# Kernel optimization log

Hardware: AMD Instinct MI355X
Metric: run time of the kernel (lower is better)

## Reference

```python
import jax, jax.numpy as jnp
import numpy as np

EPS = 1e-5

def channel_norm(x):
    # per-(batch,channel) norm over spatial dims; torch.var default is unbiased (ddof=1)
    mn = x.mean(axis=(-1, -2), keepdims=True)
    std = jnp.sqrt(x.var(axis=(-1, -2), keepdims=True, ddof=1) + EPS)
    return (x - mn) / std

def conv1x1(x, W, b):
    # x: [B,C,H,W], W: [O,C], b: [O]
    return jnp.einsum('oc,bchw->bohw', W, x) + b[None, :, None, None]

def setup_inputs() -> dict:
    key = jax.random.key(0)
    ks = jax.random.split(key, 10)
    B, C, H, W = 4, 512, 64, 64
    s = 1.0 / np.sqrt(C)  # kaiming-uniform-ish scale for 1x1 conv
    inp = {
        'f_c': jax.random.normal(ks[0], (B, C, H, W), jnp.float32),
        'f_s': jax.random.normal(ks[1], (B, C, H, W), jnp.float32),
        'W_c1': jax.random.uniform(ks[2], (C, C), jnp.float32, -s, s),
        'b_c1': jax.random.uniform(ks[3], (C,), jnp.float32, -s, s),
        'W_s1': jax.random.uniform(ks[4], (C, C), jnp.float32, -s, s),
        'b_s1': jax.random.uniform(ks[5], (C,), jnp.float32, -s, s),
        'W_s2': jax.random.uniform(ks[6], (C, C), jnp.float32, -s, s),
        'b_s2': jax.random.uniform(ks[7], (C,), jnp.float32, -s, s),
        'W_csc': jax.random.uniform(ks[8], (C, C), jnp.float32, -s, s),
        'b_csc': jax.random.uniform(ks[9], (C,), jnp.float32, -s, s),
    }
    return inp

def reference(f_c, f_s, W_c1, b_c1, W_s1, b_s1, W_s2, b_s2, W_csc, b_csc):
    B, C, H, W = f_c.shape
    f_c_hat = channel_norm(f_c)
    f_s_hat = channel_norm(f_s)
    f = conv1x1(f_c_hat, W_c1, b_c1).reshape(B, C, H * W)  # queries [B,C,N]
    g = conv1x1(f_s_hat, W_s1, b_s1).reshape(B, C, H * W)  # keys    [B,C,N]
    scores = jnp.einsum('bci,bcj->bij', f, g)              # [B,N,N]
    attention = jax.nn.softmax(scores, axis=-1)
    h = conv1x1(f_s_hat, W_s2, b_s2).reshape(B, C, H * W)  # values  [B,C,N]
    out = jnp.einsum('bcj,bij->bci', h, attention).reshape(B, C, H, W)
    return conv1x1(out, W_csc, b_csc) + f_c
```

## Files before the change

kernel.cpp:

```cpp
#include <hip/hip_runtime.h>

typedef unsigned short u16;
typedef __attribute__((ext_vector_type(8))) _Float16 f16x8;
typedef __attribute__((ext_vector_type(4))) float f32x4;
typedef __attribute__((ext_vector_type(16))) float f32x16;

#define N_SP 4096
#define C_CH 512
#define B_SZ 4

struct PtrTab { u16* p[4]; };

__device__ __forceinline__ u16 f2h(float f) {
    union { _Float16 h; u16 u; } x; x.h = (_Float16)f; return x.u;
}
__device__ __forceinline__ float h2f(u16 u) {
    union { u16 u; _Float16 h; } x; x.u = u; return (float)x.h;
}
__device__ __forceinline__ void async_cp16(const void* g, void* l) {
    __builtin_amdgcn_global_load_lds((const __attribute__((address_space(1))) unsigned*)g,
                                     (__attribute__((address_space(3))) unsigned*)l, 16, 0, 0);
}
__device__ __forceinline__ float wave_reduce_sum(float v) {
    #pragma unroll
    for (int off = 32; off; off >>= 1) v += __shfl_xor(v, off, 64);
    return v;
}
__device__ __forceinline__ float wave_reduce_max(float v) {
    #pragma unroll
    for (int off = 32; off; off >>= 1) v = fmaxf(v, __shfl_xor(v, off, 64));
    return v;
}
__device__ __forceinline__ void bar() { asm volatile("s_barrier" ::: "memory"); }
template<int N> __device__ __forceinline__ void vmwait() {
    if constexpr (N == 0)  asm volatile("s_waitcnt vmcnt(0)" ::: "memory");
    else if constexpr (N == 2)  asm volatile("s_waitcnt vmcnt(2)" ::: "memory");
    else if constexpr (N == 4)  asm volatile("s_waitcnt vmcnt(4)" ::: "memory");
    else if constexpr (N == 6)  asm volatile("s_waitcnt vmcnt(6)" ::: "memory");
    else if constexpr (N == 8)  asm volatile("s_waitcnt vmcnt(8)" ::: "memory");
}
__device__ __forceinline__ void lgkm0() {
    asm volatile("s_waitcnt lgkmcnt(0)" ::: "memory");
    __builtin_amdgcn_sched_barrier(0);
}

__global__ __launch_bounds__(256) void transpose_cast_stats(
        const float* __restrict__ fc, const float* __restrict__ fs,
        u16* __restrict__ xc, u16* __restrict__ xs,
        float* __restrict__ part_s, float* __restrict__ part_ss) {
    __shared__ float tile[64][65];
    const int t = threadIdx.x;
    const int n0 = blockIdx.x * 64, c0 = blockIdx.y * 64;
    const int z = blockIdx.z;
    const int b = z & 3, which = z >> 2;
    const float* src = which ? fs : fc;
    u16* dst = which ? xs : xc;
    const int r = t >> 4, q4 = (t & 15) * 4;
    #pragma unroll
    for (int it = 0; it < 4; ++it) {
        const int row = it * 16 + r;
        float4 v = *(const float4*)(src + ((size_t)b * C_CH + c0 + row) * N_SP + n0 + q4);
        tile[row][q4 + 0] = v.x; tile[row][q4 + 1] = v.y;
        tile[row][q4 + 2] = v.z; tile[row][q4 + 3] = v.w;
    }
    __syncthreads();
    {
        const int cr = t >> 2, q = t & 3;
        float s = 0.f, ss = 0.f;
        #pragma unroll
        for (int i = 0; i < 16; ++i) {
            float a = tile[cr][q * 16 + i];
            s += a; ss += a * a;
        }
        s += __shfl_xor(s, 1, 64);  s += __shfl_xor(s, 2, 64);
        ss += __shfl_xor(ss, 1, 64); ss += __shfl_xor(ss, 2, 64);
        if (q == 0) {
            atomicAdd(&part_s[z * 512 + c0 + cr], s);
            atomicAdd(&part_ss[z * 512 + c0 + cr], ss);
        }
    }
    #pragma unroll
    for (int it = 0; it < 4; ++it) {
        const int nrow = it * 16 + r;
        ushort4 h4;
        h4.x = f2h(tile[q4 + 0][nrow]);
        h4.y = f2h(tile[q4 + 1][nrow]);
        h4.z = f2h(tile[q4 + 2][nrow]);
        h4.w = f2h(tile[q4 + 3][nrow]);
        *(ushort4*)(dst + ((size_t)b * N_SP + n0 + nrow) * C_CH + c0 + q4) = h4;
    }
}

__global__ __launch_bounds__(256) void prep1(
        const float* __restrict__ W_c1, const float* __restrict__ W_s1,
        const float* __restrict__ W_s2, const float* __restrict__ W_csc,
        const float* __restrict__ b_c1, const float* __restrict__ b_s2,
        const float* __restrict__ b_csc,
        u16* __restrict__ Wbase,
        const float* __restrict__ part_s, const float* __restrict__ part_ss,
        float* __restrict__ mu_a, float* __restrict__ rs_a,
        float* __restrict__ w_u, float* __restrict__ bfold0) {
    __shared__ float tile[64][65];
    const int t = threadIdx.x, z = blockIdx.z;
    if (z < 4) {
        const int n0 = blockIdx.x * 64, c0 = blockIdx.y * 64;
        const float* W = (z == 0) ? W_c1 : (z == 1) ? W_s1 : (z == 2) ? W_s2 : W_csc;
        u16* D = Wbase + ((z == 0) ? 2 : (z == 1) ? 0 : (z == 2) ? 3 : 1) * 262144;
        const int r = t >> 4, q4 = (t & 15) * 4;
        #pragma unroll
        for (int it = 0; it < 4; ++it) {
            const int row = it * 16 + r;
            float4 v = *(const float4*)(W + (size_t)(c0 + row) * 512 + n0 + q4);
            if (z == 3) {
                ushort4 h4 = { f2h(v.x), f2h(v.y), f2h(v.z), f2h(v.w) };
                *(ushort4*)(D + (size_t)(c0 + row) * 512 + n0 + q4) = h4;
            } else {
                tile[row][q4 + 0] = v.x; tile[row][q4 + 1] = v.y;
                tile[row][q4 + 2] = v.z; tile[row][q4 + 3] = v.w;
            }
        }
        __syncthreads();
        if (z == 3) return;
        #pragma unroll
        for (int it = 0; it < 4; ++it) {
            const int nrow = it * 16 + r;
            ushort4 h4;
            h4.x = f2h(tile[q4 + 0][nrow]);
            h4.y = f2h(tile[q4 + 1][nrow]);
            h4.z = f2h(tile[q4 + 2][nrow]);
            h4.w = f2h(tile[q4 + 3][nrow]);
            *(ushort4*)(D + (size_t)(n0 + nrow) * 512 + c0 + q4) = h4;
        }
        return;
    }
    const int flat = blockIdx.y * 8 + blockIdx.x;
    if (flat < 8) {
        #pragma unroll
        for (int h = 0; h < 2; ++h) {
            const int c = flat * 512 + h * 256 + t;
            const float S = part_s[c], SS = part_ss[c];
            const float mean = S * (1.f / N_SP);
            const float var = (SS - S * mean) * (1.f / (N_SP - 1));
            mu_a[c] = mean;
            rs_a[c] = rsqrtf(var + 1e-5f);
        }
    } else if (flat < 10) {
        const int d = (flat - 8) * 256 + t;
        float acc = 0.f;
        for (int o = 0; o < 512; ++o) acc += b_c1[o] * W_s1[(size_t)o * 512 + d];
        w_u[d] = acc;
    } else if (flat < 42) {
        const int w4 = t >> 6, l = t & 63;
        #pragma unroll
        for (int q = 0; q < 4; ++q) {
            const int o = (flat - 10) * 16 + w4 * 4 + q;
            const float4 w0 = *(const float4*)(W_csc + (size_t)o * 512 + l * 8);
            const float4 w1 = *(const float4*)(W_csc + (size_t)o * 512 + l * 8 + 4);
            const float4 b0 = *(const float4*)(b_s2 + l * 8);
            const float4 b1 = *(const float4*)(b_s2 + l * 8 + 4);
            float acc = w0.x * b0.x + w0.y * b0.y + w0.z * b0.z + w0.w * b0.w
                      + w1.x * b1.x + w1.y * b1.y + w1.z * b1.z + w1.w * b1.w;
            acc = wave_reduce_sum(acc);
            if (l == 0) bfold0[o] = acc + b_csc[o];
        }
    }
}

__global__ __launch_bounds__(256) void prep2(
        const u16* __restrict__ WqT16, const u16* __restrict__ Wf16,
        const u16* __restrict__ xs,
        const float* __restrict__ mu_a, const float* __restrict__ rs_a,
        const float* __restrict__ bfold0, const float* __restrict__ w_u,
        u16* __restrict__ Wq_z, u16* __restrict__ Wf_z,
        float* __restrict__ bq, float* __restrict__ bh, float* __restrict__ u_) {
    const int id = blockIdx.x, t = threadIdx.x;
    if (id < 1024) {
        const int y = id >> 9;
        const size_t e = ((size_t)(id & 511) * 256 + t) * 8;
        const int z = (int)(e >> 18), rem = (int)(e & 262143);
        const int d = rem >> 9, a0 = rem & 511;
        u16 v[8];
        if (y == 0) {
            *(uint4*)v = *(const uint4*)(WqT16 + rem);
            const float rd = rs_a[(4 + z) * 512 + d];
            const float* rc = rs_a + z * 512 + a0;
            #pragma unroll
            for (int i = 0; i < 8; ++i) v[i] = f2h(h2f(v[i]) * rc[i] * rd);
            *(uint4*)(Wq_z + e) = *(const uint4*)v;
        } else {
            *(uint4*)v = *(const uint4*)(Wf16 + rem);
            const float* rk = rs_a + (4 + z) * 512 + a0;
            #pragma unroll
            for (int i = 0; i < 8; ++i) v[i] = f2h(h2f(v[i]) * rk[i]);
            *(uint4*)(Wf_z + e) = *(const uint4*)v;
        }
    } else if (id < 2048) {
        const int w = t >> 6, l = t & 63;
        const int oid = (id - 1024) * 4 + w;
        const int kind = oid >> 11;
        const int z = (oid >> 9) & 3, d = oid & 511;
        const u16* row = (kind == 0 ? WqT16 : Wf16) + (size_t)d * 512;
        const int sb = (kind == 0 ? z : 4 + z) * 512;
        float acc = 0.f;
        #pragma unroll
        for (int i = 0; i < 8; ++i) {
            const int a = l * 8 + i;
            acc += h2f(row[a]) * mu_a[sb + a] * rs_a[sb + a];
        }
        acc = wave_reduce_sum(acc);
        if (l == 0) {
            if (kind == 0) bq[z * 512 + d] = -acc * rs_a[(4 + z) * 512 + d];
            else           bh[z * 512 + d] = bfold0[d] - acc;
        }
    } else {
        const int id2 = id - 2048;
        const int b = id2 >> 6, xblk = id2 & 63;
        const int w = t >> 6, l = t & 63;
        float4 u0 = *(const float4*)(w_u + l * 8);
        float4 u1 = *(const float4*)(w_u + l * 8 + 4);
        const float4 r0 = *(const float4*)(rs_a + (4 + b) * 512 + l * 8);
        const float4 r1 = *(const float4*)(rs_a + (4 + b) * 512 + l * 8 + 4);
        u0.x *= r0.x; u0.y *= r0.y; u0.z *= r0.z; u0.w *= r0.w;
        u1.x *= r1.x; u1.y *= r1.y; u1.z *= r1.z; u1.w *= r1.w;
        #pragma unroll
        for (int jj = 0; jj < 16; ++jj) {
            const int j = xblk * 64 + w * 16 + jj;
            const u16* row = xs + ((size_t)b * N_SP + j) * C_CH + l * 8;
            f16x8 x = *(const f16x8*)row;
            float acc = (float)x[0] * u0.x + (float)x[1] * u0.y + (float)x[2] * u0.z + (float)x[3] * u0.w
                      + (float)x[4] * u1.x + (float)x[5] * u1.y + (float)x[6] * u1.z + (float)x[7] * u1.w;
            acc = wave_reduce_sum(acc);
            if (l == 0) u_[(size_t)b * N_SP + j] = acc;
        }
    }
}

enum { OUT_F32 = 0, OUT_F16 = 1 };

template<int OUTMODE, bool TABB, bool TABD, int MI, int MJ>
__global__ __launch_bounds__(256) void gemm_bt(
    const u16* __restrict__ A, const u16* __restrict__ B, PtrTab tab,
    float* __restrict__ Df, u16* __restrict__ Dh,
    const float* __restrict__ bias_m, const float* __restrict__ bias_n,
    const float* __restrict__ res,
    int M, int N, int K, int lda, int ldb, int ldd,
    size_t sA, size_t sB, size_t sD, size_t sR, int sBm, int sBn)
{
    constexpr int TM = MI * 64, TN = MJ * 64, BK = 64;
    constexpr int AITS = (TM * BK) / (256 * 8);
    constexpr int BITS = (TN * BK) / (256 * 8);
    __shared__ u16 smem[(TM + TN) * BK];
    u16* As = smem;
    u16* Bs = smem + TM * BK;

    const int t = threadIdx.x;
    const int l = t & 63, w = t >> 6;
    const int m0 = blockIdx.y * TM, n0 = blockIdx.x * TN;
    const size_t zb = blockIdx.z;
    const u16* pA = A + zb * sA + (size_t)m0 * lda;
    const u16* pB = (TABB ? tab.p[zb] : B + zb * sB) + (size_t)n0 * ldb;

    const int wr = (w & 1) * (MI * 32), wc = (w >> 1) * (MJ * 32);

    f32x16 acc[MI][MJ] = {};

    for (int k0 = 0; k0 < K; k0 += BK) {
        #pragma unroll
        for (int it = 0; it < AITS; ++it) {
            const int L = it * 256 + t;
            const int row = L >> 3, c = L & 7;
            const int sc = (c ^ (row & 7)) * 8;
            async_cp16(pA + (size_t)row * lda + k0 + sc, As + L * 8);
        }
        #pragma unroll
        for (int it = 0; it < BITS; ++it) {
            const int L = it * 256 + t;
            const int row = L >> 3, c = L & 7;
            const int sc = (c ^ (row & 7)) * 8;
            async_cp16(pB + (size_t)row * ldb + k0 + sc, Bs + L * 8);
        }
        __syncthreads();
        #pragma unroll
        for (int kk = 0; kk < 4; ++kk) {
            f16x8 af[MI], bf[MJ];
            #pragma unroll
            for (int i = 0; i < MI; ++i) {
                const int row = wr + i * 32 + (l & 31);
                const int ch = ((kk * 2 + (l >> 5)) ^ (row & 7)) * 8;
                af[i] = *(const f16x8*)(As + row * BK + ch);
            }
            #pragma unroll
            for (int j = 0; j < MJ; ++j) {
                const int row = wc + j * 32 + (l & 31);
                const int ch = ((kk * 2 + (l >> 5)) ^ (row & 7)) * 8;
                bf[j] = *(const f16x8*)(Bs + row * BK + ch);
            }
            #pragma unroll
            for (int i = 0; i < MI; ++i)
                #pragma unroll
                for (int j = 0; j < MJ; ++j)
                    acc[i][j] = __builtin_amdgcn_mfma_f32_32x32x16_f16(af[i], bf[j], acc[i][j], 0, 0, 0);
        }
        __syncthreads();
    }

    const int cl = l & 31, rh = (l >> 5) * 4;
    u16* pDh = (OUTMODE == OUT_F16) ? (TABD ? tab.p[zb] : Dh + zb * sD) : nullptr;
    float* pDf = (OUTMODE == OUT_F32) ? (Df + zb * sD) : nullptr;
    #pragma unroll
    for (int i = 0; i < MI; ++i) {
        #pragma unroll
        for (int j = 0; j < MJ; ++j) {
            const int nn = n0 + wc + j * 32 + cl;
            const float bn = bias_n ? bias_n[(size_t)sBn * zb + nn] : 0.f;
            #pragma unroll
            for (int reg = 0; reg < 16; ++reg) {
                const int ml = (reg & 3) + 8 * (reg >> 2) + rh;
                const int mm = m0 + wr + i * 32 + ml;
                float v = acc[i][j][reg] + bn;
                if (bias_m) v += bias_m[(size_t)sBm * zb + mm];
                const size_t off = (size_t)mm * ldd + nn;
                if (OUTMODE == OUT_F32) {
                    if (res) v += res[zb * sR + off];
                    pDf[off] = v;
                } else {
                    pDh[off] = f2h(v);
                }
            }
        }
    }
}

template<int OUTMODE, bool TABB, bool TABD, int BM>
__global__ __launch_bounds__(512, 2) void gemm_f(
    const u16* __restrict__ A, const u16* __restrict__ B, PtrTab tab,
    float* __restrict__ Df, u16* __restrict__ Dh,
    const float* __restrict__ bias_m, const float* __restrict__ bias_n,
    const float* __restrict__ res,
    int K, int lda, int ldb, int ldd,
    size_t sA, size_t sB, size_t sD, size_t sR, int sBm, int sBn)
{
    constexpr int BN = 256, BK = 64;
    constexpr int HM = BM / 2;
    constexpr int MF = BM / 64;
    constexpr int LA = BM / 128;
    constexpr int LB = 2;
    constexpr int LDSH = (BM + BN) * BK;
    __shared__ u16 smem[2 * LDSH];

    const int t = threadIdx.x;
    const int l = t & 63, w = t >> 6;
    const int m0 = blockIdx.y * BM, n0 = blockIdx.x * BN;
    const size_t zb = blockIdx.z;
    const u16* pA = A + zb * sA + (size_t)m0 * lda;
    const u16* pB = (TABB ? tab.p[zb] : B + zb * sB) + (size_t)n0 * ldb;

    const int wr = (w & 1) * (HM / 2);
    const int wc = (w >> 1) * 32;

    f32x4 acc[2 * MF][4] = {};

    auto stageA = [&](int buf, int k0, int half) {
        u16* dst = smem + buf * LDSH;
        #pragma unroll
        for (int it = 0; it < LA; ++it) {
            const int L = it * 512 + t;
            const int row = half * HM + (L >> 3), c = L & 7;
            const int sc = (c ^ (row & 7)) * 8;
            async_cp16(pA + (size_t)row * lda + k0 + sc, dst + row * BK + c * 8);
        }
    };
    auto stageB = [&](int buf, int k0, int half) {
        u16* dst = smem + buf * LDSH + BM * BK;
        #pragma unroll
        for (int it = 0; it < LB; ++it) {
            const int L = it * 512 + t;
            const int row = half * 128 + (L >> 3), c = L & 7;
            const int sc = (c ^ (row & 7)) * 8;
            async_cp16(pB + (size_t)row * ldb + k0 + sc, dst + row * BK + c * 8);
        }
    };
    auto rdA = [&](const u16* As, int qi, int mf, int kk) -> f16x8 {
        const int row = qi * HM + wr + mf * 16 + (l & 15);
        const int ch = (kk * 4 + (l >> 4)) ^ (row & 7);
        return *(const f16x8*)(As + row * BK + ch * 8);
    };
    auto rdB = [&](const u16* Bs, int qj, int nf, int kk) -> f16x8 {
        const int row = qj * 128 + wc + nf * 16 + (l & 15);
        const int ch = (kk * 4 + (l >> 4)) ^ (row & 7);
        return *(const f16x8*)(Bs + row * BK + ch * 8);
    };

    f16x8 af[2][MF][2];
    f16x8 bf[2][2];

    const int NT = K / BK;
    stageA(0, 0, 0); stageA(0, 0, 1); stageB(0, 0, 0); stageB(0, 0, 1);
    vmwait<LB>();
    bar();

    for (int tl = 0; tl < NT; ++tl) {
        const int cur = tl & 1, nxt = cur ^ 1;
        const u16* As = smem + cur * LDSH;
        const u16* Bs = As + BM * BK;
        const int k1 = (tl + 1) * BK;
        const bool pf = (tl + 1 < NT);

        #pragma unroll
        for (int mf = 0; mf < MF; ++mf) { af[0][mf][0] = rdA(As, 0, mf, 0); af[0][mf][1] = rdA(As, 0, mf, 1); }
        #pragma unroll
        for (int nf = 0; nf < 2; ++nf) { bf[nf][0] = rdB(Bs, 0, nf, 0); bf[nf][1] = rdB(Bs, 0, nf, 1); }
        if (pf) stageA(nxt, k1, 0);
        lgkm0();
        __builtin_amdgcn_s_setprio(1);
        #pragma unroll
        for (int mf = 0; mf < MF; ++mf)
            #pragma unroll
            for (int nf = 0; nf < 2; ++nf) {
                acc[mf][nf] = __builtin_amdgcn_mfma_f32_16x16x32_f16(af[0][mf][0], bf[nf][0], acc[mf][nf], 0, 0, 0);
                acc[mf][nf] = __builtin_amdgcn_mfma_f32_16x16x32_f16(af[0][mf][1], bf[nf][1], acc[mf][nf], 0, 0, 0);
            }
        __builtin_amdgcn_s_setprio(0);
        bar();

        #pragma unroll
        for (int mf = 0; mf < MF; ++mf) { af[1][mf][0] = rdA(As, 1, mf, 0); af[1][mf][1] = rdA(As, 1, mf, 1); }
        if (pf) stageA(nxt, k1, 1);
        lgkm0();
        __builtin_amdgcn_s_setprio(1);
        #pragma unroll
        for (int mf = 0; mf < MF; ++mf)
            #pragma unroll
            for (int nf = 0; nf < 2; ++nf) {
                acc[MF + mf][nf] = __builtin_amdgcn_mfma_f32_16x16x32_f16(af[1][mf][0], bf[nf][0], acc[MF + mf][nf], 0, 0, 0);
                acc[MF + mf][nf] = __builtin_amdgcn_mfma_f32_16x16x32_f16(af[1][mf][1], bf[nf][1], acc[MF + mf][nf], 0, 0, 0);
            }
        __builtin_amdgcn_s_setprio(0);
        if (pf) vmwait<2 * LA>(); else vmwait<0>();
        bar();

        #pragma unroll
        for (int nf = 0; nf < 2; ++nf) { bf[nf][0] = rdB(Bs, 1, nf, 0); bf[nf][1] = rdB(Bs, 1, nf, 1); }
        if (pf) stageB(nxt, k1, 0);
        lgkm0();
        __builtin_amdgcn_s_setprio(1);
        #pragma unroll
        for (int mf = 0; mf < MF; ++mf)
            #pragma unroll
            for (int nf = 0; nf < 2; ++nf) {
                acc[MF + mf][2 + nf] = __builtin_amdgcn_mfma_f32_16x16x32_f16(af[1][mf][0], bf[nf][0], acc[MF + mf][2 + nf], 0, 0, 0);
                acc[MF + mf][2 + nf] = __builtin_amdgcn_mfma_f32_16x16x32_f16(af[1][mf][1], bf[nf][1], acc[MF + mf][2 + nf], 0, 0, 0);
            }
        __builtin_amdgcn_s_setprio(0);
        bar();

        if (pf) stageB(nxt, k1, 1);
        __builtin_amdgcn_s_setprio(1);
        #pragma unroll
        for (int mf = 0; mf < MF; ++mf)
            #pragma unroll
            for (int nf = 0; nf < 2; ++nf) {
                acc[mf][2 + nf] = __builtin_amdgcn_mfma_f32_16x16x32_f16(af[0][mf][0], bf[nf][0], acc[mf][2 + nf], 0, 0, 0);
                acc[mf][2 + nf] = __builtin_amdgcn_mfma_f32_16x16x32_f16(af[0][mf][1], bf[nf][1], acc[mf][2 + nf], 0, 0, 0);
            }
        __builtin_amdgcn_s_setprio(0);
        if (pf) vmwait<LB>();
        bar();
    }

    const int cl = l & 15, rh = (l >> 4) * 4;
    u16* pDh = (OUTMODE == OUT_F16) ? (TABD ? tab.p[zb] : Dh + zb * sD) : nullptr;
    float* pDf = (OUTMODE == OUT_F32) ? (Df + zb * sD) : nullptr;
    #pragma unroll
    for (int qi = 0; qi < 2; ++qi) {
        #pragma unroll
        for (int qj = 0; qj < 2; ++qj) {
            #pragma unroll
            for (int mf = 0; mf < MF; ++mf) {
                #pragma unroll
                for (int nf = 0; nf < 2; ++nf) {
                    const int nn = n0 + qj * 128 + wc + nf * 16 + cl;
                    const float bn = bias_n ? bias_n[(size_t)sBn * zb + nn] : 0.f;
                    const f32x4 a4 = acc[qi * MF + mf][qj * 2 + nf];
                    #pragma unroll
                    for (int reg = 0; reg < 4; ++reg) {
                        const int mm = m0 + qi * HM + wr + mf * 16 + rh + reg;
                        float v = a4[reg] + bn;
                        if (bias_m) v += bias_m[(size_t)sBm * zb + mm];
                        const size_t off = (size_t)mm * ldd + nn;
                        if (OUTMODE == OUT_F32) {
                            if (res) v += res[zb * sR + off];
                            pDf[off] = v;
                        } else {
                            pDh[off] = f2h(v);
                        }
                    }
                }
            }
        }
    }
}

__global__ __launch_bounds__(256) void softmax_kernel(PtrTab tab) {
    u16* row = tab.p[blockIdx.y] + (size_t)blockIdx.x * N_SP;
    const int t = threadIdx.x;
    u16 raw[16];
    *(uint4*)(raw + 0) = *(const uint4*)(row + t * 16);
    *(uint4*)(raw + 8) = *(const uint4*)(row + t * 16 + 8);
    float v[16];
    float mx = -1e30f;
    #pragma unroll
    for (int i = 0; i < 16; ++i) { v[i] = h2f(raw[i]); mx = fmaxf(mx, v[i]); }
    mx = wave_reduce_max(mx);
    __shared__ float red[4];
    const int wave = t >> 6;
    if ((t & 63) == 0) red[wave] = mx;
    __syncthreads();
    mx = fmaxf(fmaxf(red[0], red[1]), fmaxf(red[2], red[3]));
    float sum = 0.f;
    #pragma unroll
    for (int i = 0; i < 16; ++i) { v[i] = __expf(v[i] - mx); sum += v[i]; }
    sum = wave_reduce_sum(sum);
    __syncthreads();
    if ((t & 63) == 0) red[wave] = sum;
    __syncthreads();
    const float inv = 1.f / (red[0] + red[1] + red[2] + red[3]);
    #pragma unroll
    for (int i = 0; i < 16; ++i) raw[i] = f2h(v[i] * inv);
    *(uint4*)(row + t * 16)     = *(const uint4*)(raw + 0);
    *(uint4*)(row + t * 16 + 8) = *(const uint4*)(raw + 8);
}

extern "C" void kernel_launch(void* const* d_in, const int* in_sizes, int n_in,
                              void* d_out, int out_size, void* d_ws, size_t ws_size,
                              hipStream_t stream) {
    const float* f_c   = (const float*)d_in[0];
    const float* f_s   = (const float*)d_in[1];
    const float* W_c1  = (const float*)d_in[2];
    const float* b_c1  = (const float*)d_in[3];
    const float* W_s1  = (const float*)d_in[4];
    const float* b_s1  = (const float*)d_in[5]; (void)b_s1;
    const float* W_s2  = (const float*)d_in[6];
    const float* b_s2  = (const float*)d_in[7];
    const float* W_csc = (const float*)d_in[8];
    const float* b_csc = (const float*)d_in[9];

    const size_t PB = (size_t)N_SP * C_CH;
    const size_t M1 = 1024 * 1024;

    u16* ws   = (u16*)d_ws;
    u16* Xs   = ws;
    u16* q_   = ws + 8 * M1;
    u16* hc   = ws + 16 * M1;
    u16* Xc   = ws + 24 * M1;
    u16* S3   = ws + 24 * M1;
    u16* S0   = ws + 40 * M1;
    u16* S1   = ws + 56 * M1;
    u16* S2   = ws + 72 * M1;
    u16* Wbase= ws + 88 * M1;
    u16* WqT16= Wbase + 4 * 262144;
    u16* Wf16 = Wbase + 5 * 262144;
    u16* Wq_z = Wbase + 6 * 262144;
    u16* Wf_z = Wq_z + 1048576;
    float* f32b = (float*)(ws + 92 * M1);
    float* part_s  = f32b;
    float* part_ss = f32b + 4096;
    float* mu_a    = f32b + 8192;
    float* rs_a    = f32b + 12288;
    float* w_u     = f32b + 16384;
    float* bfold0  = f32b + 16896;
    float* bq      = f32b + 17408;
    float* bh      = f32b + 19456;
    float* u_      = f32b + 21504;

    PtrTab Stab; Stab.p[0] = S0; Stab.p[1] = S1; Stab.p[2] = S2; Stab.p[3] = S3;
    PtrTab tab0 = Stab;

    hipMemsetAsync(part_s, 0, 2 * 4096 * sizeof(float), stream);

    transpose_cast_stats<<<dim3(64, 8, 8), 256, 0, stream>>>(f_c, f_s, Xc, Xs, part_s, part_ss);

    prep1<<<dim3(8, 8, 5), 256, 0, stream>>>(W_c1, W_s1, W_s2, W_csc, b_c1, b_s2, b_csc,
                                             Wbase, part_s, part_ss, mu_a, rs_a, w_u, bfold0);

    gemm_bt<OUT_F16, false, false, 2, 2><<<dim3(4, 4, 2), 256, 0, stream>>>(
        Wbase, Wbase + 2 * 262144, tab0, nullptr, WqT16, nullptr, nullptr, nullptr,
        512, 512, 512, 512, 512, 512, 262144, 262144, 262144, 0, 0, 0);

    prep2<<<2304, 256, 0, stream>>>(WqT16, Wf16, Xs, mu_a, rs_a, bfold0, w_u,
                                    Wq_z, Wf_z, bq, bh, u_);

    gemm_f<OUT_F16, false, false, 128><<<dim3(2, 32, B_SZ), 512, 0, stream>>>(
        Xc, Wq_z, tab0, nullptr, q_, nullptr, bq, nullptr,
        C_CH, C_CH, C_CH, C_CH, PB, 262144, PB, 0, 0, 512);
    gemm_f<OUT_F16, false, false, 128><<<dim3(16, 4, B_SZ), 512, 0, stream>>>(
        Wf_z, Xs, tab0, nullptr, hc, bh, nullptr, nullptr,
        C_CH, C_CH, C_CH, N_SP, 262144, PB, PB, 0, 512, 0);

    gemm_f<OUT_F16, false, true, 128><<<dim3(16, 32, B_SZ), 512, 0, stream>>>(
        q_, Xs, Stab, nullptr, nullptr, nullptr, u_, nullptr,
        C_CH, C_CH, C_CH, N_SP, PB, PB, 0, 0, 0, N_SP);

    softmax_kernel<<<dim3(N_SP, B_SZ), 256, 0, stream>>>(Stab);

    gemm_f<OUT_F32, true, false, 128><<<dim3(16, 4, B_SZ), 512, 0, stream>>>(
        hc, nullptr, Stab, (float*)d_out, nullptr, nullptr, nullptr, f_c,
        N_SP, N_SP, N_SP, N_SP, PB, 0, PB, PB, 0, 0);
}
```

Baseline: 448.5 us.

## Add 128x256 GEMM variant for small-M GEMMs and enlarge score GEMM tile

Adds a new gemm_f2 kernel with a 128x256 block tile and a two-phase K loop that reuses A fragments across both column halves of the tile. The Q projection, value projection and final P·V GEMMs now use it. The score GEMM switches to a 256-row M tile, which halves its grid in the M dimension. The aim is more data reuse per block and fewer blocks. The cost is higher register pressure and fewer blocks, which can leave CUs underfilled on the smaller grids.

```diff
diff --git a/kernel.cpp b/kernel.cpp
--- a/kernel.cpp
+++ b/kernel.cpp
@@ -465,6 +465,155 @@
             }
         __builtin_amdgcn_s_setprio(0);
         if (pf) vmwait<LB>();
+        bar();
+    }
+
+    const int cl = l & 15, rh = (l >> 4) * 4;
+    u16* pDh = (OUTMODE == OUT_F16) ? (TABD ? tab.p[zb] : Dh + zb * sD) : nullptr;
+    float* pDf = (OUTMODE == OUT_F32) ? (Df + zb * sD) : nullptr;
+    #pragma unroll
+    for (int qi = 0; qi < 2; ++qi) {
+        #pragma unroll
+        for (int qj = 0; qj < 2; ++qj) {
+            #pragma unroll
+            for (int mf = 0; mf < MF; ++mf) {
+                #pragma unroll
+                for (int nf = 0; nf < 2; ++nf) {
+                    const int nn = n0 + qj * 128 + wc + nf * 16 + cl;
+                    const float bn = bias_n ? bias_n[(size_t)sBn * zb + nn] : 0.f;
+                    const f32x4 a4 = acc[qi * MF + mf][qj * 2 + nf];
+                    #pragma unroll
+                    for (int reg = 0; reg < 4; ++reg) {
+                        const int mm = m0 + qi * HM + wr + mf * 16 + rh + reg;
+                        float v = a4[reg] + bn;
+                        if (bias_m) v += bias_m[(size_t)sBm * zb + mm];
+                        const size_t off = (size_t)mm * ldd + nn;
+                        if (OUTMODE == OUT_F32) {
+                            if (res) v += res[zb * sR + off];
+                            pDf[off] = v;
+                        } else {
+                            pDh[off] = f2h(v);
+                        }
+                    }
+                }
+            }
+        }
+    }
+}
+
+template<int OUTMODE, bool TABB, bool TABD>
+__global__ __launch_bounds__(512, 2) void gemm_f2(
+    const u16* __restrict__ A, const u16* __restrict__ B, PtrTab tab,
+    float* __restrict__ Df, u16* __restrict__ Dh,
+    const float* __restrict__ bias_m, const float* __restrict__ bias_n,
+    const float* __restrict__ res,
+    int K, int lda, int ldb, int ldd,
+    size_t sA, size_t sB, size_t sD, size_t sR, int sBm, int sBn)
+{
+    constexpr int BM = 128, BN = 256, BK = 64;
+    constexpr int HM = 64, MF = 2, LA = 1, LB = 2;
+    constexpr int LDSH = (BM + BN) * BK;
+    __shared__ u16 smem[2 * LDSH];
+
+    const int t = threadIdx.x;
+    const int l = t & 63, w = t >> 6;
+    const int m0 = blockIdx.y * BM, n0 = blockIdx.x * BN;
+    const size_t zb = blockIdx.z;
+    const u16* pA = A + zb * sA + (size_t)m0 * lda;
+    const u16* pB = (TABB ? tab.p[zb] : B + zb * sB) + (size_t)n0 * ldb;
+
+    const int wr = (w & 1) * (HM / 2);
+    const int wc = (w >> 1) * 32;
+
+    f32x4 acc[2 * MF][4] = {};
+
+    auto stageA = [&](int buf, int k0, int half) {
+        u16* dst = smem + buf * LDSH;
+        #pragma unroll
+        for (int it = 0; it < LA; ++it) {
+            const int L = it * 512 + t;
+            const int row = half * HM + (L >> 3), c = L & 7;
+            const int sc = (c ^ (row & 7)) * 8;
+            async_cp16(pA + (size_t)row * lda + k0 + sc, dst + row * BK + c * 8);
+        }
+    };
+    auto stageB = [&](int buf, int k0, int half) {
+        u16* dst = smem + buf * LDSH + BM * BK;
+        #pragma unroll
+        for (int it = 0; it < LB; ++it) {
+            const int L = it * 512 + t;
+            const int row = half * 128 + (L >> 3), c = L & 7;
+            const int sc = (c ^ (row & 7)) * 8;
+            async_cp16(pB + (size_t)row * ldb + k0 + sc, dst + row * BK + c * 8);
+        }
+    };
+    auto rdA = [&](const u16* As, int qi, int mf, int kk) -> f16x8 {
+        const int row = qi * HM + wr + mf * 16 + (l & 15);
+        const int ch = (kk * 4 + (l >> 4)) ^ (row & 7);
+        return *(const f16x8*)(As + row * BK + ch * 8);
+    };
+    auto rdB = [&](const u16* Bs, int qj, int nf, int kk) -> f16x8 {
+        const int row = qj * 128 + wc + nf * 16 + (l & 15);
+        const int ch = (kk * 4 + (l >> 4)) ^ (row & 7);
+        return *(const f16x8*)(Bs + row * BK + ch * 8);
+    };
+
+    f16x8 af[2][MF][2];
+    f16x8 bf[2][2];
+
+    const int NT = K / BK;
+    stageA(0, 0, 0); stageA(0, 0, 1); stageB(0, 0, 0); stageB(0, 0, 1);
+    vmwait<2>();
+    bar();
+
+    for (int tl = 0; tl < NT; ++tl) {
+        const int cur = tl & 1, nxt = cur ^ 1;
+        const u16* As = smem + cur * LDSH;
+        const u16* Bs = As + BM * BK;
+        const int k1 = (tl + 1) * BK;
+        const bool pf = (tl + 1 < NT);
+
+        #pragma unroll
+        for (int qi = 0; qi < 2; ++qi)
+            #pragma unroll
+            for (int mf = 0; mf < MF; ++mf) {
+                af[qi][mf][0] = rdA(As, qi, mf, 0);
+                af[qi][mf][1] = rdA(As, qi, mf, 1);
+            }
+        #pragma unroll
+        for (int nf = 0; nf < 2; ++nf) { bf[nf][0] = rdB(Bs, 0, nf, 0); bf[nf][1] = rdB(Bs, 0, nf, 1); }
+        if (pf) { stageA(nxt, k1, 0); stageA(nxt, k1, 1); stageB(nxt, k1, 0); }
+        lgkm0();
+        __builtin_amdgcn_s_setprio(1);
+        #pragma unroll
+        for (int qi = 0; qi < 2; ++qi)
+            #pragma unroll
+            for (int mf = 0; mf < MF; ++mf)
+                #pragma unroll
+                for (int nf = 0; nf < 2; ++nf) {
+                    acc[qi * MF + mf][nf] = __builtin_amdgcn_mfma_f32_16x16x32_f16(af[qi][mf][0], bf[nf][0], acc[qi * MF + mf][nf], 0, 0, 0);
+                    acc[qi * MF + mf][nf] = __builtin_amdgcn_mfma_f32_16x16x32_f16(af[qi][mf][1], bf[nf][1], acc[qi * MF + mf][nf], 0, 0, 0);
+                }
+        __builtin_amdgcn_s_setprio(0);
+        if (pf) vmwait<4>(); else vmwait<0>();
+        bar();
+
+        #pragma unroll
+        for (int nf = 0; nf < 2; ++nf) { bf[nf][0] = rdB(Bs, 1, nf, 0); bf[nf][1] = rdB(Bs, 1, nf, 1); }
+        if (pf) stageB(nxt, k1, 1);
+        lgkm0();
+        __builtin_amdgcn_s_setprio(1);
+        #pragma unroll
+        for (int qi = 0; qi < 2; ++qi)
+            #pragma unroll
+            for (int mf = 0; mf < MF; ++mf)
+                #pragma unroll
+                for (int nf = 0; nf < 2; ++nf) {
+                    acc[qi * MF + mf][2 + nf] = __builtin_amdgcn_mfma_f32_16x16x32_f16(af[qi][mf][0], bf[nf][0], acc[qi * MF + mf][2 + nf], 0, 0, 0);
+                    acc[qi * MF + mf][2 + nf] = __builtin_amdgcn_mfma_f32_16x16x32_f16(af[qi][mf][1], bf[nf][1], acc[qi * MF + mf][2 + nf], 0, 0, 0);
+                }
+        __builtin_amdgcn_s_setprio(0);
+        if (pf) vmwait<2>();
         bar();
     }
 
@@ -590,20 +739,20 @@
     prep2<<<2304, 256, 0, stream>>>(WqT16, Wf16, Xs, mu_a, rs_a, bfold0, w_u,
                                     Wq_z, Wf_z, bq, bh, u_);
 
-    gemm_f<OUT_F16, false, false, 128><<<dim3(2, 32, B_SZ), 512, 0, stream>>>(
+    gemm_f2<OUT_F16, false, false><<<dim3(2, 32, B_SZ), 512, 0, stream>>>(
         Xc, Wq_z, tab0, nullptr, q_, nullptr, bq, nullptr,
         C_CH, C_CH, C_CH, C_CH, PB, 262144, PB, 0, 0, 512);
-    gemm_f<OUT_F16, false, false, 128><<<dim3(16, 4, B_SZ), 512, 0, stream>>>(
+    gemm_f2<OUT_F16, false, false><<<dim3(16, 4, B_SZ), 512, 0, stream>>>(
         Wf_z, Xs, tab0, nullptr, hc, bh, nullptr, nullptr,
         C_CH, C_CH, C_CH, N_SP, 262144, PB, PB, 0, 512, 0);
 
-    gemm_f<OUT_F16, false, true, 128><<<dim3(16, 32, B_SZ), 512, 0, stream>>>(
+    gemm_f<OUT_F16, false, true, 256><<<dim3(16, 16, B_SZ), 512, 0, stream>>>(
         q_, Xs, Stab, nullptr, nullptr, nullptr, u_, nullptr,
         C_CH, C_CH, C_CH, N_SP, PB, PB, 0, 0, 0, N_SP);
 
     softmax_kernel<<<dim3(N_SP, B_SZ), 256, 0, stream>>>(Stab);
 
-    gemm_f<OUT_F32, true, false, 128><<<dim3(16, 4, B_SZ), 512, 0, stream>>>(
+    gemm_f2<OUT_F32, true, false><<<dim3(16, 4, B_SZ), 512, 0, stream>>>(
         hc, nullptr, Stab, (float*)d_out, nullptr, nullptr, nullptr, f_c,
         N_SP, N_SP, N_SP, N_SP, PB, 0, PB, PB, 0, 0);
 }
```

After: 423.5 us. 5.6% less time.

## Reschedule GEMM main loop with double-buffered B fragments and larger score tile

Applied to the files above, without the earlier changes.

Restructures the MFMA main loop so both A quadrants are read up front and B fragments live in two separate register sets. This removes the explicit lgkmcnt(0) waits and sched barriers, so LDS reads can overlap with MFMA issue, and the vmcnt wait moves to an earlier phase. Separately, the score GEMM now uses a 256-row tile with half as many blocks along M. The costs are higher register pressure and possibly lower occupancy. The earlier vmwait and the new barrier placement also risk subtle LDS ordering issues.

```diff
diff --git a/kernel.cpp b/kernel.cpp
--- a/kernel.cpp
+++ b/kernel.cpp
@@ -34,14 +34,11 @@
 __device__ __forceinline__ void bar() { asm volatile("s_barrier" ::: "memory"); }
 template<int N> __device__ __forceinline__ void vmwait() {
     if constexpr (N == 0)  asm volatile("s_waitcnt vmcnt(0)" ::: "memory");
+    else if constexpr (N == 1)  asm volatile("s_waitcnt vmcnt(1)" ::: "memory");
     else if constexpr (N == 2)  asm volatile("s_waitcnt vmcnt(2)" ::: "memory");
     else if constexpr (N == 4)  asm volatile("s_waitcnt vmcnt(4)" ::: "memory");
     else if constexpr (N == 6)  asm volatile("s_waitcnt vmcnt(6)" ::: "memory");
     else if constexpr (N == 8)  asm volatile("s_waitcnt vmcnt(8)" ::: "memory");
-}
-__device__ __forceinline__ void lgkm0() {
-    asm volatile("s_waitcnt lgkmcnt(0)" ::: "memory");
-    __builtin_amdgcn_sched_barrier(0);
 }
 
 __global__ __launch_bounds__(256) void transpose_cast_stats(
@@ -392,7 +389,8 @@
     };
 
     f16x8 af[2][MF][2];
-    f16x8 bf[2][2];
+    f16x8 bf0[2][2];
+    f16x8 bf1[2][2];
 
     const int NT = K / BK;
     stageA(0, 0, 0); stageA(0, 0, 1); stageB(0, 0, 0); stageB(0, 0, 1);
@@ -409,47 +407,44 @@
         #pragma unroll
         for (int mf = 0; mf < MF; ++mf) { af[0][mf][0] = rdA(As, 0, mf, 0); af[0][mf][1] = rdA(As, 0, mf, 1); }
         #pragma unroll
-        for (int nf = 0; nf < 2; ++nf) { bf[nf][0] = rdB(Bs, 0, nf, 0); bf[nf][1] = rdB(Bs, 0, nf, 1); }
+        for (int nf = 0; nf < 2; ++nf) { bf0[nf][0] = rdB(Bs, 0, nf, 0); bf0[nf][1] = rdB(Bs, 0, nf, 1); }
+        #pragma unroll
+        for (int mf = 0; mf < MF; ++mf) { af[1][mf][0] = rdA(As, 1, mf, 0); af[1][mf][1] = rdA(As, 1, mf, 1); }
         if (pf) stageA(nxt, k1, 0);
-        lgkm0();
         __builtin_amdgcn_s_setprio(1);
         #pragma unroll
         for (int mf = 0; mf < MF; ++mf)
             #pragma unroll
             for (int nf = 0; nf < 2; ++nf) {
-                acc[mf][nf] = __builtin_amdgcn_mfma_f32_16x16x32_f16(af[0][mf][0], bf[nf][0], acc[mf][nf], 0, 0, 0);
-                acc[mf][nf] = __builtin_amdgcn_mfma_f32_16x16x32_f16(af[0][mf][1], bf[nf][1], acc[mf][nf], 0, 0, 0);
+                acc[mf][nf] = __builtin_amdgcn_mfma_f32_16x16x32_f16(af[0][mf][0], bf0[nf][0], acc[mf][nf], 0, 0, 0);
+                acc[mf][nf] = __builtin_amdgcn_mfma_f32_16x16x32_f16(af[0][mf][1], bf0[nf][1], acc[mf][nf], 0, 0, 0);
+            }
+        __builtin_amdgcn_s_setprio(0);
+        if (pf) vmwait<LA>(); else vmwait<0>();
+        bar();
+
+        #pragma unroll
+        for (int nf = 0; nf < 2; ++nf) { bf1[nf][0] = rdB(Bs, 1, nf, 0); bf1[nf][1] = rdB(Bs, 1, nf, 1); }
+        if (pf) stageA(nxt, k1, 1);
+        __builtin_amdgcn_s_setprio(1);
+        #pragma unroll
+        for (int mf = 0; mf < MF; ++mf)
+            #pragma unroll
+            for (int nf = 0; nf < 2; ++nf) {
+                acc[MF + mf][nf] = __builtin_amdgcn_mfma_f32_16x16x32_f16(af[1][mf][0], bf0[nf][0], acc[MF + mf][nf], 0, 0, 0);
+                acc[MF + mf][nf] = __builtin_amdgcn_mfma_f32_16x16x32_f16(af[1][mf][1], bf0[nf][1], acc[MF + mf][nf], 0, 0, 0);
             }
         __builtin_amdgcn_s_setprio(0);
         bar();
 
-        #pragma unroll
-        for (int mf = 0; mf < MF; ++mf) { af[1][mf][0] = rdA(As, 1, mf, 0); af[1][mf][1] = rdA(As, 1, mf, 1); }
-        if (pf) stageA(nxt, k1, 1);
-        lgkm0();
+        if (pf) stageB(nxt, k1, 0);
         __builtin_amdgcn_s_setprio(1);
         #pragma unroll
         for (int mf = 0; mf < MF; ++mf)
             #pragma unroll
             for (int nf = 0; nf < 2; ++nf) {
-                acc[MF + mf][nf] = __builtin_amdgcn_mfma_f32_16x16x32_f16(af[1][mf][0], bf[nf][0], acc[MF + mf][nf], 0, 0, 0);
-                acc[MF + mf][nf] = __builtin_amdgcn_mfma_f32_16x16x32_f16(af[1][mf][1], bf[nf][1], acc[MF + mf][nf], 0, 0, 0);
-            }
-        __builtin_amdgcn_s_setprio(0);
-        if (pf) vmwait<2 * LA>(); else vmwait<0>();
-        bar();
-
-        #pragma unroll
-        for (int nf = 0; nf < 2; ++nf) { bf[nf][0] = rdB(Bs, 1, nf, 0); bf[nf][1] = rdB(Bs, 1, nf, 1); }
-        if (pf) stageB(nxt, k1, 0);
-        lgkm0();
-        __builtin_amdgcn_s_setprio(1);
-        #pragma unroll
-        for (int mf = 0; mf < MF; ++mf)
-            #pragma unroll
-            for (int nf = 0; nf < 2; ++nf) {
-                acc[MF + mf][2 + nf] = __builtin_amdgcn_mfma_f32_16x16x32_f16(af[1][mf][0], bf[nf][0], acc[MF + mf][2 + nf], 0, 0, 0);
-                acc[MF + mf][2 + nf] = __builtin_amdgcn_mfma_f32_16x16x32_f16(af[1][mf][1], bf[nf][1], acc[MF + mf][2 + nf], 0, 0, 0);
+                acc[MF + mf][2 + nf] = __builtin_amdgcn_mfma_f32_16x16x32_f16(af[1][mf][0], bf1[nf][0], acc[MF + mf][2 + nf], 0, 0, 0);
+                acc[MF + mf][2 + nf] = __builtin_amdgcn_mfma_f32_16x16x32_f16(af[1][mf][1], bf1[nf][1], acc[MF + mf][2 + nf], 0, 0, 0);
             }
         __builtin_amdgcn_s_setprio(0);
         bar();
@@ -460,8 +455,8 @@
         for (int mf = 0; mf < MF; ++mf)
             #pragma unroll
             for (int nf = 0; nf < 2; ++nf) {
-                acc[mf][2 + nf] = __builtin_amdgcn_mfma_f32_16x16x32_f16(af[0][mf][0], bf[nf][0], acc[mf][2 + nf], 0, 0, 0);
-                acc[mf][2 + nf] = __builtin_amdgcn_mfma_f32_16x16x32_f16(af[0][mf][1], bf[nf][1], acc[mf][2 + nf], 0, 0, 0);
+                acc[mf][2 + nf] = __builtin_amdgcn_mfma_f32_16x16x32_f16(af[0][mf][0], bf1[nf][0], acc[mf][2 + nf], 0, 0, 0);
+                acc[mf][2 + nf] = __builtin_amdgcn_mfma_f32_16x16x32_f16(af[0][mf][1], bf1[nf][1], acc[mf][2 + nf], 0, 0, 0);
             }
         __builtin_amdgcn_s_setprio(0);
         if (pf) vmwait<LB>();
@@ -597,7 +592,7 @@
         Wf_z, Xs, tab0, nullptr, hc, bh, nullptr, nullptr,
         C_CH, C_CH, C_CH, N_SP, 262144, PB, PB, 0, 512, 0);
 
-    gemm_f<OUT_F16, false, true, 128><<<dim3(16, 32, B_SZ), 512, 0, stream>>>(
+    gemm_f<OUT_F16, false, true, 256><<<dim3(16, 16, B_SZ), 512, 0, stream>>>(
         q_, Xs, Stab, nullptr, nullptr, nullptr, u_, nullptr,
         C_CH, C_CH, C_CH, N_SP, PB, PB, 0, 0, 0, N_SP);
 
```

Result: faster. 439.1 us (-2.1%).
